# Kernel tuning notes

Measured on AMD Instinct MI355X. Metric: run time of the kernel, lower is better.

The kernel has to match this reference:

```python
import jax, jax.numpy as jnp
import numpy as np

NPOINT = 1024
RADIUS = 0.2
NSAMPLE = 64
BN_EPS = 1e-5


def setup_inputs() -> dict:
    key = jax.random.key(0)
    ks = jax.random.split(key, 16)
    B, N = 8, 8192
    inp = {
        "xyz": jax.random.normal(ks[0], (B, 3, N), jnp.float32),
        "points": jax.random.normal(ks[1], (B, 3, N), jnp.float32),
        "seed_inds": jax.random.randint(ks[2], (B, N), 0, N),
    }
    chans = [6, 64, 64, 128]
    for i in range(3):
        cin, cout = chans[i], chans[i + 1]
        kk = jax.random.split(ks[3 + i], 3)
        inp[f"w{i}"] = jax.random.normal(kk[0], (cout, cin), jnp.float32) / np.sqrt(cin)
        inp[f"b{i}"] = jnp.zeros((cout,), jnp.float32)
        inp[f"g{i}"] = jnp.ones((cout,), jnp.float32)
        inp[f"be{i}"] = jnp.zeros((cout,), jnp.float32)
        inp[f"m{i}"] = jax.random.normal(kk[1], (cout,), jnp.float32) * 0.1
        inp[f"v{i}"] = jax.random.uniform(kk[2], (cout,), jnp.float32, 0.5, 1.5)
    return inp


def _fps(xyz, npoint):
    # xyz: [B, N, 3]. Deterministic start at index 0 (torch uses a random start).
    B, N, _ = xyz.shape

    def step(carry, _):
        dist, far = carry
        cent = jnp.take_along_axis(xyz, far[:, None, None], axis=1)  # [B,1,3]
        d = jnp.sum((xyz - cent) ** 2, -1)                           # [B,N]
        dist = jnp.minimum(dist, d)
        nxt = jnp.argmax(dist, -1)
        return (dist, nxt), far

    init = (jnp.full((B, N), 1e10, xyz.dtype), jnp.zeros((B,), jnp.int32))
    _, idxs = jax.lax.scan(step, init, None, length=npoint)
    return idxs.T  # [B, npoint]


def _sqdist(src, dst):
    # src [B,S,3], dst [B,N,3] -> [B,S,N]
    d = -2.0 * jnp.einsum("bsc,bnc->bsn", src, dst)
    d += jnp.sum(src ** 2, -1)[:, :, None]
    d += jnp.sum(dst ** 2, -1)[:, None, :]
    return d


def _gather(pts, idx):
    # pts [B,N,C], idx [B,S,K] -> [B,S,K,C]
    B, S, K = idx.shape
    flat = jnp.take_along_axis(pts, idx.reshape(B, S * K, 1), axis=1)
    return flat.reshape(B, S, K, pts.shape[-1])


def _forward(xyz, points, seed_inds, layers):
    xyz_t = xyz.transpose(0, 2, 1)      # [B,N,3]
    pts_t = points.transpose(0, 2, 1)   # [B,N,D]
    B, N, _ = xyz_t.shape

    fps_idx = _fps(xyz_t, NPOINT)                                   # [B,S]
    new_seed = jnp.take_along_axis(seed_inds, fps_idx.astype(seed_inds.dtype), axis=1)
    new_xyz = jnp.take_along_axis(xyz_t, fps_idx[:, :, None], axis=1)  # [B,S,3]

    # ball query via sort trick (same math as torch module)
    sq = _sqdist(new_xyz, xyz_t)                                    # [B,S,N]
    gi = jnp.where(sq > RADIUS ** 2, N, jnp.arange(N, dtype=jnp.int32)[None, None, :])
    gi = jnp.sort(gi, axis=-1)[:, :, :NSAMPLE]                      # [B,S,K]
    first = gi[:, :, :1]
    gi = jnp.where(gi == N, first, gi)

    gxyz = _gather(xyz_t, gi) - new_xyz[:, :, None, :]              # [B,S,K,3]
    gpts = _gather(pts_t, gi)                                       # [B,S,K,D]
    feat = jnp.concatenate([gxyz, gpts], -1)                        # [B,S,K,3+D]

    for (w, b, g, be, m, v) in layers:
        feat = jnp.einsum("bskc,oc->bsko", feat, w) + b             # 1x1 conv
        feat = (feat - m) * (g / jnp.sqrt(v + BN_EPS)) + be         # BN (inference)
        feat = jax.nn.relu(feat)

    new_points = jnp.max(feat, axis=2).transpose(0, 2, 1)           # [B,Cout,S]
    return new_xyz.transpose(0, 2, 1), new_points, new_seed


def reference(xyz, points, seed_inds,
              w0, b0, g0, be0, m0, v0,
              w1, b1, g1, be1, m1, v1,
              w2, b2, g2, be2, m2, v2):
    layers = [(w0, b0, g0, be0, m0, v0),
              (w1, b1, g1, be1, m1, v1),
              (w2, b2, g2, be2, m2, v2)]
    return _forward(xyz, points, seed_inds, layers)
```

## Files before the change

kernel.cpp:

```cpp
#include <hip/hip_runtime.h>

#define B_ 8
#define N_ 8192
#define S_ 1024
#define NS_ 64

typedef float v2f __attribute__((ext_vector_type(2)));
typedef unsigned long long u64;

#define OUT0 0
#define OUT1 24576
#define OUT2 1073152

template <int CTRL>
static __device__ __forceinline__ float dpp_max_step(float v) {
    int o = __builtin_amdgcn_update_dpp(__float_as_int(v), __float_as_int(v),
                                        CTRL, 0xf, 0xf, false);
    return fmaxf(v, __int_as_float(o));
}
static __device__ __forceinline__ float wave_max_to_lane63(float v) {
    v = dpp_max_step<0x111>(v);
    v = dpp_max_step<0x112>(v);
    v = dpp_max_step<0x114>(v);
    v = dpp_max_step<0x118>(v);
    v = dpp_max_step<0x142>(v);
    v = dpp_max_step<0x143>(v);
    return v;
}
static __device__ __forceinline__ float wave_max_f32(float v) {
    v = wave_max_to_lane63(v);
    return __int_as_float(__builtin_amdgcn_readlane(__float_as_int(v), 63));
}
template <int CTRL>
static __device__ __forceinline__ unsigned dpp_umin_step(unsigned v) {
    unsigned o = (unsigned)__builtin_amdgcn_update_dpp((int)v, (int)v,
                                                       CTRL, 0xf, 0xf, false);
    return v < o ? v : o;
}
static __device__ __forceinline__ unsigned wave_min_u32(unsigned v) {
    v = dpp_umin_step<0x111>(v);
    v = dpp_umin_step<0x112>(v);
    v = dpp_umin_step<0x114>(v);
    v = dpp_umin_step<0x118>(v);
    v = dpp_umin_step<0x142>(v);
    v = dpp_umin_step<0x143>(v);
    return (unsigned)__builtin_amdgcn_readlane((int)v, 63);
}

#define FPS_T 512
#define FPS_J 8

__global__ __launch_bounds__(FPS_T, 1) void fps_kernel(const float* __restrict__ xyz,
                                                       float* out) {
    const int b = blockIdx.x;
    const int t = threadIdx.x;
    const int lane = t & 63;
    const float* X = xyz + b * 3 * N_;

    v2f px2[FPS_J], py2[FPS_J], pz2[FPS_J], dist2[FPS_J];
#pragma unroll
    for (int j = 0; j < FPS_J; ++j) {
        int n = t + 1024 * j;
        px2[j] = (v2f){X[n], X[n + 512]};
        py2[j] = (v2f){X[N_ + n], X[N_ + n + 512]};
        pz2[j] = (v2f){X[2 * N_ + n], X[2 * N_ + n + 512]};
        dist2[j] = (v2f){1e10f, 1e10f};
    }

    __shared__ u64 pairs[2];
    if (t == 0) { pairs[0] = 0ull; pairs[1] = 0ull; }
    __syncthreads();

    float* oseed = out + OUT2 + b * S_;

    int ci = 0;
    float c0 = X[0], c1 = X[N_], c2 = X[2 * N_];

    for (int step = 0; step < S_; ++step) {
        if (t == 0) oseed[step] = __int_as_float(ci);

        v2f mv = (v2f){-1.0f, -1.0f};
        {
#pragma clang fp contract(off)
            v2f c0v = (v2f){c0, c0};
            v2f c1v = (v2f){c1, c1};
            v2f c2v = (v2f){c2, c2};
#pragma unroll
            for (int j = 0; j < FPS_J; ++j) {
                v2f e0 = px2[j] - c0v;
                v2f e1 = py2[j] - c1v;
                v2f e2 = pz2[j] - c2v;
                v2f q0 = e0 * e0;
                v2f q1 = e1 * e1;
                v2f q2 = e2 * e2;
                v2f d  = (q0 + q1) + q2;
                v2f dm = __builtin_elementwise_min(dist2[j], d);
                dist2[j] = dm;
                mv = __builtin_elementwise_max(mv, dm);
            }
        }
        float m = fmaxf(mv.x, mv.y);

        float wmax = wave_max_f32(m);

        unsigned mask = 0u;
#pragma unroll
        for (int j = 0; j < FPS_J; ++j) {
            if (dist2[j].x == wmax) mask |= (1u << (2 * j));
            if (dist2[j].y == wmax) mask |= (1u << (2 * j + 1));
        }
        unsigned cand = 0xffffffffu;
        if (mask) {
            int bit = __ffs(mask) - 1;
            cand = (unsigned)(t + (bit << 9));
        }
        unsigned widx = wave_min_u32(cand);

        if (lane == 0) {
            u64 pv = ((u64)(step + 1) << 45) |
                     ((u64)__float_as_uint(wmax) << 13) |
                     (u64)(8191u - widx);
            atomicMax(&pairs[(step + 1) & 1], pv);
        }
        __syncthreads();

        u64 p = pairs[(step + 1) & 1];
        ci = 8191 - (int)(p & 0x1fffull);
        int cu = __builtin_amdgcn_readfirstlane(ci);
        c0 = X[cu];
        c1 = X[N_ + cu];
        c2 = X[2 * N_ + cu];
    }
}

__global__ __launch_bounds__(256) void gather_kernel(const float* __restrict__ xyz,
                                                     const int* __restrict__ seed,
                                                     float* out) {
    int t = blockIdx.x * 256 + threadIdx.x;
    int b = t >> 10, s = t & 1023;
    int idx = __float_as_int(out[OUT2 + t]) & 8191;
    const float* X = xyz + b * 3 * N_;
    float x = X[idx], y = X[N_ + idx], z = X[2 * N_ + idx];
    out[OUT0 + (b * 3 + 0) * S_ + s] = x;
    out[OUT0 + (b * 3 + 1) * S_ + s] = y;
    out[OUT0 + (b * 3 + 2) * S_ + s] = z;
    out[OUT2 + t] = (float)seed[b * N_ + idx];
}

__global__ __launch_bounds__(256) void ballquery_kernel(const float* __restrict__ xyz,
                                                        float* out) {
    int wid = threadIdx.x >> 6, lane = threadIdx.x & 63;
    int sg = blockIdx.x * 4 + wid;
    int b = sg >> 10, s = sg & 1023;
    const float* X = xyz + b * 3 * N_;
    float c0 = out[OUT0 + (b * 3 + 0) * S_ + s];
    float c1 = out[OUT0 + (b * 3 + 1) * S_ + s];
    float c2 = out[OUT0 + (b * 3 + 2) * S_ + s];
    float* G = out + OUT1 + (b * 128) * S_ + s;

    int cnt = 0, first = 0;
    for (int base = 0; base < N_ && cnt < NS_; base += 128) {
        int n0 = base + lane;
        int n1 = base + 64 + lane;
        float x0 = X[n0], y0 = X[N_ + n0], z0 = X[2 * N_ + n0];
        float x1 = X[n1], y1 = X[N_ + n1], z1 = X[2 * N_ + n1];
        float e0 = x0 - c0, e1 = y0 - c1, e2 = z0 - c2;
        float d0 = fmaf(e2, e2, fmaf(e1, e1, e0 * e0));
        float f0 = x1 - c0, f1 = y1 - c1, f2 = z1 - c2;
        float d1 = fmaf(f2, f2, fmaf(f1, f1, f0 * f0));

        u64 mask0 = __ballot(d0 <= 0.04f);
        if (mask0) {
            if (cnt == 0) first = base + __ffsll(mask0) - 1;
            int pos = cnt + (int)__popcll(mask0 & ((1ull << lane) - 1ull));
            if ((d0 <= 0.04f) && pos < NS_) G[pos * S_] = __int_as_float(n0);
            cnt += (int)__popcll(mask0);
        }
        u64 mask1 = __ballot(d1 <= 0.04f);
        if (mask1) {
            if (cnt == 0) first = base + 64 + __ffsll(mask1) - 1;
            int pos = cnt + (int)__popcll(mask1 & ((1ull << lane) - 1ull));
            if ((d1 <= 0.04f) && pos < NS_) G[pos * S_] = __int_as_float(n1);
            cnt += (int)__popcll(mask1);
        }
    }
    if (lane >= cnt && lane < NS_) G[lane * S_] = __int_as_float(first);
}

__global__ __launch_bounds__(256) void mlp_kernel(
    const float* __restrict__ xyz, const float* __restrict__ pts,
    const float* __restrict__ w0, const float* __restrict__ b0,
    const float* __restrict__ g0, const float* __restrict__ be0,
    const float* __restrict__ m0, const float* __restrict__ v0,
    const float* __restrict__ w1, const float* __restrict__ b1,
    const float* __restrict__ g1, const float* __restrict__ be1,
    const float* __restrict__ m1, const float* __restrict__ v1,
    const float* __restrict__ w2, const float* __restrict__ b2,
    const float* __restrict__ g2, const float* __restrict__ be2,
    const float* __restrict__ m2, const float* __restrict__ v2,
    float* out) {
    const int sg = blockIdx.x;
    const int b = sg >> 10, s = sg & 1023;
    const int t = threadIdx.x;
    const int lane = t & 63;
    const int wq = __builtin_amdgcn_readfirstlane(t >> 6);

    __shared__ float f0[64 * 9];
    __shared__ float bufA[64 * 65];
    __shared__ float bufB[64 * 65];
    __shared__ float scs[256], ofs[256];

    {
        float sc, of;
        if (t < 64) {
            int c = t;
            sc = g0[c] / sqrtf(v0[c] + 1e-5f);
            of = (b0[c] - m0[c]) * sc + be0[c];
        } else if (t < 128) {
            int c = t - 64;
            sc = g1[c] / sqrtf(v1[c] + 1e-5f);
            of = (b1[c] - m1[c]) * sc + be1[c];
        } else {
            int c = t - 128;
            sc = g2[c] / sqrtf(v2[c] + 1e-5f);
            of = (b2[c] - m2[c]) * sc + be2[c];
        }
        scs[t] = sc;
        ofs[t] = of;
    }

    if (t < 64) {
        int gidx = __float_as_int(out[OUT1 + (b * 128 + t) * S_ + s]) & 8191;
        const float* X = xyz + b * 3 * N_;
        const float* P = pts + b * 3 * N_;
        float cx = out[OUT0 + (b * 3 + 0) * S_ + s];
        float cy = out[OUT0 + (b * 3 + 1) * S_ + s];
        float cz = out[OUT0 + (b * 3 + 2) * S_ + s];
        f0[t * 9 + 0] = X[gidx] - cx;
        f0[t * 9 + 1] = X[N_ + gidx] - cy;
        f0[t * 9 + 2] = X[2 * N_ + gidx] - cz;
        f0[t * 9 + 3] = P[gidx];
        f0[t * 9 + 4] = P[N_ + gidx];
        f0[t * 9 + 5] = P[2 * N_ + gidx];
    }
    __syncthreads();

    {
        float in[6];
#pragma unroll
        for (int c = 0; c < 6; ++c) in[c] = f0[lane * 9 + c];
#pragma unroll 1
        for (int i = 0; i < 16; i += 4) {
            int o = wq * 16 + i;
            float a0 = 0.f, a1 = 0.f, a2 = 0.f, a3 = 0.f;
#pragma unroll
            for (int c = 0; c < 6; ++c) {
                float rc = in[c];
                a0 = fmaf(rc, w0[(o + 0) * 6 + c], a0);
                a1 = fmaf(rc, w0[(o + 1) * 6 + c], a1);
                a2 = fmaf(rc, w0[(o + 2) * 6 + c], a2);
                a3 = fmaf(rc, w0[(o + 3) * 6 + c], a3);
            }
            bufA[lane * 65 + o + 0] = fmaxf(fmaf(a0, scs[o + 0], ofs[o + 0]), 0.f);
            bufA[lane * 65 + o + 1] = fmaxf(fmaf(a1, scs[o + 1], ofs[o + 1]), 0.f);
            bufA[lane * 65 + o + 2] = fmaxf(fmaf(a2, scs[o + 2], ofs[o + 2]), 0.f);
            bufA[lane * 65 + o + 3] = fmaxf(fmaf(a3, scs[o + 3], ofs[o + 3]), 0.f);
        }
    }
    __syncthreads();

    {
        float r[64];
#pragma unroll
        for (int c = 0; c < 64; ++c) r[c] = bufA[lane * 65 + c];
#pragma unroll 1
        for (int i = 0; i < 16; i += 4) {
            int o = wq * 16 + i;
            float a0 = 0.f, a1 = 0.f, a2 = 0.f, a3 = 0.f;
#pragma unroll
            for (int c = 0; c < 64; ++c) {
                float rc = r[c];
                a0 = fmaf(rc, w1[(o + 0) * 64 + c], a0);
                a1 = fmaf(rc, w1[(o + 1) * 64 + c], a1);
                a2 = fmaf(rc, w1[(o + 2) * 64 + c], a2);
                a3 = fmaf(rc, w1[(o + 3) * 64 + c], a3);
            }
            bufB[lane * 65 + o + 0] = fmaxf(fmaf(a0, scs[64 + o + 0], ofs[64 + o + 0]), 0.f);
            bufB[lane * 65 + o + 1] = fmaxf(fmaf(a1, scs[64 + o + 1], ofs[64 + o + 1]), 0.f);
            bufB[lane * 65 + o + 2] = fmaxf(fmaf(a2, scs[64 + o + 2], ofs[64 + o + 2]), 0.f);
            bufB[lane * 65 + o + 3] = fmaxf(fmaf(a3, scs[64 + o + 3], ofs[64 + o + 3]), 0.f);
        }
    }
    __syncthreads();

    {
        float r[64];
#pragma unroll
        for (int c = 0; c < 64; ++c) r[c] = bufB[lane * 65 + c];
#pragma unroll 1
        for (int i = 0; i < 32; i += 4) {
            int o = wq * 32 + i;
            float a0 = 0.f, a1 = 0.f, a2 = 0.f, a3 = 0.f;
#pragma unroll
            for (int c = 0; c < 64; ++c) {
                float rc = r[c];
                a0 = fmaf(rc, w2[(o + 0) * 64 + c], a0);
                a1 = fmaf(rc, w2[(o + 1) * 64 + c], a1);
                a2 = fmaf(rc, w2[(o + 2) * 64 + c], a2);
                a3 = fmaf(rc, w2[(o + 3) * 64 + c], a3);
            }
            float y0 = wave_max_to_lane63(fmaxf(fmaf(a0, scs[128 + o + 0], ofs[128 + o + 0]), 0.f));
            float y1 = wave_max_to_lane63(fmaxf(fmaf(a1, scs[128 + o + 1], ofs[128 + o + 1]), 0.f));
            float y2 = wave_max_to_lane63(fmaxf(fmaf(a2, scs[128 + o + 2], ofs[128 + o + 2]), 0.f));
            float y3 = wave_max_to_lane63(fmaxf(fmaf(a3, scs[128 + o + 3], ofs[128 + o + 3]), 0.f));
            if (lane == 63) {
                out[OUT1 + (b * 128 + o + 0) * S_ + s] = y0;
                out[OUT1 + (b * 128 + o + 1) * S_ + s] = y1;
                out[OUT1 + (b * 128 + o + 2) * S_ + s] = y2;
                out[OUT1 + (b * 128 + o + 3) * S_ + s] = y3;
            }
        }
    }
}

extern "C" void kernel_launch(void* const* d_in, const int* in_sizes, int n_in,
                              void* d_out, int out_size, void* d_ws, size_t ws_size,
                              hipStream_t stream) {
    const float* xyz  = (const float*)d_in[0];
    const float* pts  = (const float*)d_in[1];
    const int*   seed = (const int*)d_in[2];
    const float* w0 = (const float*)d_in[3];
    const float* b0 = (const float*)d_in[4];
    const float* g0 = (const float*)d_in[5];
    const float* be0 = (const float*)d_in[6];
    const float* m0 = (const float*)d_in[7];
    const float* v0 = (const float*)d_in[8];
    const float* w1 = (const float*)d_in[9];
    const float* b1 = (const float*)d_in[10];
    const float* g1 = (const float*)d_in[11];
    const float* be1 = (const float*)d_in[12];
    const float* m1 = (const float*)d_in[13];
    const float* v1 = (const float*)d_in[14];
    const float* w2 = (const float*)d_in[15];
    const float* b2 = (const float*)d_in[16];
    const float* g2 = (const float*)d_in[17];
    const float* be2 = (const float*)d_in[18];
    const float* m2 = (const float*)d_in[19];
    const float* v2 = (const float*)d_in[20];
    float* out = (float*)d_out;
    (void)d_ws; (void)ws_size;

    fps_kernel<<<dim3(B_), dim3(FPS_T), 0, stream>>>(xyz, out);
    gather_kernel<<<dim3(8192 / 256), dim3(256), 0, stream>>>(xyz, seed, out);
    ballquery_kernel<<<dim3(2048), dim3(256), 0, stream>>>(xyz, out);
    mlp_kernel<<<dim3(8192), dim3(256), 0, stream>>>(xyz, pts,
        w0, b0, g0, be0, m0, v0,
        w1, b1, g1, be1, m1, v1,
        w2, b2, g2, be2, m2, v2,
        out);
}
```

Baseline: 1.433 ms.

## Fuse FPS, ball query and MLP into one persistent kernel with flag-based overlap

Adds a persistent fused kernel in which 8 blocks run farthest point sampling and publish progress through release/acquire flags every 64 centroids. The other 248 blocks poll those flags and do ball query, gather and the 3-layer MLP for each finished centroid, so this work overlaps the long serial FPS phase instead of waiting for it. FPS now writes centroid coordinates directly, which removes the separate gather kernel. The design relies on all 256 blocks being co-resident and on workspace being available; otherwise it falls back to the multi-kernel path.

Result: slower. 2.639 ms (+84.2%).

```diff
diff --git a/kernel.cpp b/kernel.cpp
--- a/kernel.cpp
+++ b/kernel.cpp
@@ -50,6 +50,280 @@
 #define FPS_T 512
 #define FPS_J 8
 
+__global__ __launch_bounds__(512, 1) void fused_kernel(
+    const float* __restrict__ xyz, const float* __restrict__ pts,
+    const int* __restrict__ seed,
+    const float* __restrict__ w0, const float* __restrict__ b0,
+    const float* __restrict__ g0, const float* __restrict__ be0,
+    const float* __restrict__ m0, const float* __restrict__ v0,
+    const float* __restrict__ w1, const float* __restrict__ b1,
+    const float* __restrict__ g1, const float* __restrict__ be1,
+    const float* __restrict__ m1, const float* __restrict__ v1,
+    const float* __restrict__ w2, const float* __restrict__ b2,
+    const float* __restrict__ g2, const float* __restrict__ be2,
+    const float* __restrict__ m2, const float* __restrict__ v2,
+    float* out, int* flags) {
+
+    __shared__ u64 pairs[2];
+    __shared__ float f0[64 * 9];
+    __shared__ float bufA[64 * 65];
+    __shared__ float bufB[64 * 65];
+    __shared__ float scs[256], ofs[256];
+    __shared__ int gis[64];
+
+    const int t = threadIdx.x;
+    const int lane = t & 63;
+
+    if (blockIdx.x < 8) {
+        const int b = blockIdx.x;
+        const float* X = xyz + b * 3 * N_;
+
+        v2f px2[FPS_J], py2[FPS_J], pz2[FPS_J], dist2[FPS_J];
+#pragma unroll
+        for (int j = 0; j < FPS_J; ++j) {
+            int n = t + 1024 * j;
+            px2[j] = (v2f){X[n], X[n + 512]};
+            py2[j] = (v2f){X[N_ + n], X[N_ + n + 512]};
+            pz2[j] = (v2f){X[2 * N_ + n], X[2 * N_ + n + 512]};
+            dist2[j] = (v2f){1e10f, 1e10f};
+        }
+
+        if (t == 0) { pairs[0] = 0ull; pairs[1] = 0ull; }
+        __syncthreads();
+
+        float* oseed = out + OUT2 + b * S_;
+
+        int ci = 0;
+        float c0 = X[0], c1 = X[N_], c2 = X[2 * N_];
+
+        for (int step = 0; step < S_; ++step) {
+            if (t == 0) oseed[step] = __int_as_float(ci);
+            if (t < 3) {
+                float cv = (t == 0) ? c0 : (t == 1) ? c1 : c2;
+                out[OUT0 + (b * 3 + t) * S_ + step] = cv;
+            }
+
+            v2f mv = (v2f){-1.0f, -1.0f};
+            {
+#pragma clang fp contract(off)
+                v2f c0v = (v2f){c0, c0};
+                v2f c1v = (v2f){c1, c1};
+                v2f c2v = (v2f){c2, c2};
+#pragma unroll
+                for (int j = 0; j < FPS_J; ++j) {
+                    v2f e0 = px2[j] - c0v;
+                    v2f e1 = py2[j] - c1v;
+                    v2f e2 = pz2[j] - c2v;
+                    v2f q0 = e0 * e0;
+                    v2f q1 = e1 * e1;
+                    v2f q2 = e2 * e2;
+                    v2f d  = (q0 + q1) + q2;
+                    v2f dm = __builtin_elementwise_min(dist2[j], d);
+                    dist2[j] = dm;
+                    mv = __builtin_elementwise_max(mv, dm);
+                }
+            }
+            float m = fmaxf(mv.x, mv.y);
+            float wmax = wave_max_f32(m);
+
+            unsigned mask = 0u;
+#pragma unroll
+            for (int j = 0; j < FPS_J; ++j) {
+                if (dist2[j].x == wmax) mask |= (1u << (2 * j));
+                if (dist2[j].y == wmax) mask |= (1u << (2 * j + 1));
+            }
+            unsigned cand = 0xffffffffu;
+            if (mask) {
+                int bit = __ffs(mask) - 1;
+                cand = (unsigned)(t + (bit << 9));
+            }
+            unsigned widx = wave_min_u32(cand);
+
+            if (lane == 0) {
+                u64 pv = ((u64)(step + 1) << 45) |
+                         ((u64)__float_as_uint(wmax) << 13) |
+                         (u64)(8191u - widx);
+                atomicMax(&pairs[(step + 1) & 1], pv);
+            }
+            __syncthreads();
+
+            u64 p = pairs[(step + 1) & 1];
+            ci = 8191 - (int)(p & 0x1fffull);
+            int cu = __builtin_amdgcn_readfirstlane(ci);
+            c0 = X[cu];
+            c1 = X[N_ + cu];
+            c2 = X[2 * N_ + cu];
+
+            if ((step & 63) == 63 && t == 0) {
+                __hip_atomic_store(&flags[b], step + 1, __ATOMIC_RELEASE,
+                                   __HIP_MEMORY_SCOPE_AGENT);
+            }
+        }
+    } else {
+        const int wq = __builtin_amdgcn_readfirstlane(t >> 6);
+
+        if (t < 256) {
+            float sc, of;
+            if (t < 64) {
+                int c = t;
+                sc = g0[c] / sqrtf(v0[c] + 1e-5f);
+                of = (b0[c] - m0[c]) * sc + be0[c];
+            } else if (t < 128) {
+                int c = t - 64;
+                sc = g1[c] / sqrtf(v1[c] + 1e-5f);
+                of = (b1[c] - m1[c]) * sc + be1[c];
+            } else {
+                int c = t - 128;
+                sc = g2[c] / sqrtf(v2[c] + 1e-5f);
+                of = (b2[c] - m2[c]) * sc + be2[c];
+            }
+            scs[t] = sc;
+            ofs[t] = of;
+        }
+        __syncthreads();
+
+        for (int sg = (int)blockIdx.x - 8; sg < B_ * S_; sg += 248) {
+            const int b = sg >> 10, s = sg & 1023;
+            const int want = s + 1;
+
+            while (__hip_atomic_load(&flags[b], __ATOMIC_ACQUIRE,
+                                     __HIP_MEMORY_SCOPE_AGENT) < want) {
+                __builtin_amdgcn_s_sleep(8);
+            }
+            __syncthreads();
+
+            const float* X = xyz + b * 3 * N_;
+            float cx = out[OUT0 + (b * 3 + 0) * S_ + s];
+            float cy = out[OUT0 + (b * 3 + 1) * S_ + s];
+            float cz = out[OUT0 + (b * 3 + 2) * S_ + s];
+
+            if (t < 64) {
+                int cnt = 0, first = 0;
+                for (int base = 0; base < N_ && cnt < NS_; base += 128) {
+                    int n0 = base + lane;
+                    int n1 = base + 64 + lane;
+                    float x0 = X[n0], y0 = X[N_ + n0], z0 = X[2 * N_ + n0];
+                    float x1 = X[n1], y1 = X[N_ + n1], z1 = X[2 * N_ + n1];
+                    float e0 = x0 - cx, e1 = y0 - cy, e2 = z0 - cz;
+                    float d0 = fmaf(e2, e2, fmaf(e1, e1, e0 * e0));
+                    float q0 = x1 - cx, q1 = y1 - cy, q2 = z1 - cz;
+                    float d1 = fmaf(q2, q2, fmaf(q1, q1, q0 * q0));
+
+                    u64 m0b = __ballot(d0 <= 0.04f);
+                    if (m0b) {
+                        if (cnt == 0) first = base + __ffsll(m0b) - 1;
+                        int pos = cnt + (int)__popcll(m0b & ((1ull << lane) - 1ull));
+                        if ((d0 <= 0.04f) && pos < NS_) gis[pos] = n0;
+                        cnt += (int)__popcll(m0b);
+                    }
+                    u64 m1b = __ballot(d1 <= 0.04f);
+                    if (m1b) {
+                        if (cnt == 0) first = base + 64 + __ffsll(m1b) - 1;
+                        int pos = cnt + (int)__popcll(m1b & ((1ull << lane) - 1ull));
+                        if ((d1 <= 0.04f) && pos < NS_) gis[pos] = n1;
+                        cnt += (int)__popcll(m1b);
+                    }
+                }
+                if (lane >= cnt && lane < NS_) gis[lane] = first;
+            } else if (t == 64) {
+                int sidx = __float_as_int(out[OUT2 + b * S_ + s]) & 8191;
+                out[OUT2 + b * S_ + s] = (float)seed[b * N_ + sidx];
+            }
+            __syncthreads();
+
+            if (t < 64) {
+                int gidx = gis[t] & 8191;
+                const float* P = pts + b * 3 * N_;
+                f0[t * 9 + 0] = X[gidx] - cx;
+                f0[t * 9 + 1] = X[N_ + gidx] - cy;
+                f0[t * 9 + 2] = X[2 * N_ + gidx] - cz;
+                f0[t * 9 + 3] = P[gidx];
+                f0[t * 9 + 4] = P[N_ + gidx];
+                f0[t * 9 + 5] = P[2 * N_ + gidx];
+            }
+            __syncthreads();
+
+            {
+                float in[6];
+#pragma unroll
+                for (int c = 0; c < 6; ++c) in[c] = f0[lane * 9 + c];
+#pragma unroll 1
+                for (int i = 0; i < 8; i += 4) {
+                    int o = wq * 8 + i;
+                    float a0 = 0.f, a1 = 0.f, a2 = 0.f, a3 = 0.f;
+#pragma unroll
+                    for (int c = 0; c < 6; ++c) {
+                        float rc = in[c];
+                        a0 = fmaf(rc, w0[(o + 0) * 6 + c], a0);
+                        a1 = fmaf(rc, w0[(o + 1) * 6 + c], a1);
+                        a2 = fmaf(rc, w0[(o + 2) * 6 + c], a2);
+                        a3 = fmaf(rc, w0[(o + 3) * 6 + c], a3);
+                    }
+                    bufA[lane * 65 + o + 0] = fmaxf(fmaf(a0, scs[o + 0], ofs[o + 0]), 0.f);
+                    bufA[lane * 65 + o + 1] = fmaxf(fmaf(a1, scs[o + 1], ofs[o + 1]), 0.f);
+                    bufA[lane * 65 + o + 2] = fmaxf(fmaf(a2, scs[o + 2], ofs[o + 2]), 0.f);
+                    bufA[lane * 65 + o + 3] = fmaxf(fmaf(a3, scs[o + 3], ofs[o + 3]), 0.f);
+                }
+            }
+            __syncthreads();
+
+            {
+                float r[64];
+#pragma unroll
+                for (int c = 0; c < 64; ++c) r[c] = bufA[lane * 65 + c];
+#pragma unroll 1
+                for (int i = 0; i < 8; i += 4) {
+                    int o = wq * 8 + i;
+                    float a0 = 0.f, a1 = 0.f, a2 = 0.f, a3 = 0.f;
+#pragma unroll
+                    for (int c = 0; c < 64; ++c) {
+                        float rc = r[c];
+                        a0 = fmaf(rc, w1[(o + 0) * 64 + c], a0);
+                        a1 = fmaf(rc, w1[(o + 1) * 64 + c], a1);
+                        a2 = fmaf(rc, w1[(o + 2) * 64 + c], a2);
+                        a3 = fmaf(rc, w1[(o + 3) * 64 + c], a3);
+                    }
+                    bufB[lane * 65 + o + 0] = fmaxf(fmaf(a0, scs[64 + o + 0], ofs[64 + o + 0]), 0.f);
+                    bufB[lane * 65 + o + 1] = fmaxf(fmaf(a1, scs[64 + o + 1], ofs[64 + o + 1]), 0.f);
+                    bufB[lane * 65 + o + 2] = fmaxf(fmaf(a2, scs[64 + o + 2], ofs[64 + o + 2]), 0.f);
+                    bufB[lane * 65 + o + 3] = fmaxf(fmaf(a3, scs[64 + o + 3], ofs[64 + o + 3]), 0.f);
+                }
+            }
+            __syncthreads();
+
+            {
+                float r[64];
+#pragma unroll
+                for (int c = 0; c < 64; ++c) r[c] = bufB[lane * 65 + c];
+#pragma unroll 1
+                for (int i = 0; i < 16; i += 4) {
+                    int o = wq * 16 + i;
+                    float a0 = 0.f, a1 = 0.f, a2 = 0.f, a3 = 0.f;
+#pragma unroll
+                    for (int c = 0; c < 64; ++c) {
+                        float rc = r[c];
+                        a0 = fmaf(rc, w2[(o + 0) * 64 + c], a0);
+                        a1 = fmaf(rc, w2[(o + 1) * 64 + c], a1);
+                        a2 = fmaf(rc, w2[(o + 2) * 64 + c], a2);
+                        a3 = fmaf(rc, w2[(o + 3) * 64 + c], a3);
+                    }
+                    float y0 = wave_max_to_lane63(fmaxf(fmaf(a0, scs[128 + o + 0], ofs[128 + o + 0]), 0.f));
+                    float y1 = wave_max_to_lane63(fmaxf(fmaf(a1, scs[128 + o + 1], ofs[128 + o + 1]), 0.f));
+                    float y2 = wave_max_to_lane63(fmaxf(fmaf(a2, scs[128 + o + 2], ofs[128 + o + 2]), 0.f));
+                    float y3 = wave_max_to_lane63(fmaxf(fmaf(a3, scs[128 + o + 3], ofs[128 + o + 3]), 0.f));
+                    if (lane == 63) {
+                        out[OUT1 + (b * 128 + o + 0) * S_ + s] = y0;
+                        out[OUT1 + (b * 128 + o + 1) * S_ + s] = y1;
+                        out[OUT1 + (b * 128 + o + 2) * S_ + s] = y2;
+                        out[OUT1 + (b * 128 + o + 3) * S_ + s] = y3;
+                    }
+                }
+            }
+            __syncthreads();
+        }
+    }
+}
+
 __global__ __launch_bounds__(FPS_T, 1) void fps_kernel(const float* __restrict__ xyz,
                                                        float* out) {
     const int b = blockIdx.x;
@@ -66,19 +340,18 @@
         pz2[j] = (v2f){X[2 * N_ + n], X[2 * N_ + n + 512]};
         dist2[j] = (v2f){1e10f, 1e10f};
     }
-
     __shared__ u64 pairs[2];
     if (t == 0) { pairs[0] = 0ull; pairs[1] = 0ull; }
     __syncthreads();
-
     float* oseed = out + OUT2 + b * S_;
-
     int ci = 0;
     float c0 = X[0], c1 = X[N_], c2 = X[2 * N_];
-
     for (int step = 0; step < S_; ++step) {
         if (t == 0) oseed[step] = __int_as_float(ci);
-
+        if (t < 3) {
+            float cv = (t == 0) ? c0 : (t == 1) ? c1 : c2;
+            out[OUT0 + (b * 3 + t) * S_ + step] = cv;
+        }
         v2f mv = (v2f){-1.0f, -1.0f};
         {
 #pragma clang fp contract(off)
@@ -100,9 +373,7 @@
             }
         }
         float m = fmaxf(mv.x, mv.y);
-
         float wmax = wave_max_f32(m);
-
         unsigned mask = 0u;
 #pragma unroll
         for (int j = 0; j < FPS_J; ++j) {
@@ -115,7 +386,6 @@
             cand = (unsigned)(t + (bit << 9));
         }
         unsigned widx = wave_min_u32(cand);
-
         if (lane == 0) {
             u64 pv = ((u64)(step + 1) << 45) |
                      ((u64)__float_as_uint(wmax) << 13) |
@@ -123,7 +393,6 @@
             atomicMax(&pairs[(step + 1) & 1], pv);
         }
         __syncthreads();
-
         u64 p = pairs[(step + 1) & 1];
         ci = 8191 - (int)(p & 0x1fffull);
         int cu = __builtin_amdgcn_readfirstlane(ci);
@@ -133,17 +402,11 @@
     }
 }
 
-__global__ __launch_bounds__(256) void gather_kernel(const float* __restrict__ xyz,
-                                                     const int* __restrict__ seed,
-                                                     float* out) {
+__global__ __launch_bounds__(256) void seedconv_kernel(const int* __restrict__ seed,
+                                                       float* out) {
     int t = blockIdx.x * 256 + threadIdx.x;
-    int b = t >> 10, s = t & 1023;
+    int b = t >> 10;
     int idx = __float_as_int(out[OUT2 + t]) & 8191;
-    const float* X = xyz + b * 3 * N_;
-    float x = X[idx], y = X[N_ + idx], z = X[2 * N_ + idx];
-    out[OUT0 + (b * 3 + 0) * S_ + s] = x;
-    out[OUT0 + (b * 3 + 1) * S_ + s] = y;
-    out[OUT0 + (b * 3 + 2) * S_ + s] = z;
     out[OUT2 + t] = (float)seed[b * N_ + idx];
 }
 
@@ -157,7 +420,6 @@
     float c1 = out[OUT0 + (b * 3 + 1) * S_ + s];
     float c2 = out[OUT0 + (b * 3 + 2) * S_ + s];
     float* G = out + OUT1 + (b * 128) * S_ + s;
-
     int cnt = 0, first = 0;
     for (int base = 0; base < N_ && cnt < NS_; base += 128) {
         int n0 = base + lane;
@@ -166,22 +428,21 @@
         float x1 = X[n1], y1 = X[N_ + n1], z1 = X[2 * N_ + n1];
         float e0 = x0 - c0, e1 = y0 - c1, e2 = z0 - c2;
         float d0 = fmaf(e2, e2, fmaf(e1, e1, e0 * e0));
-        float f0 = x1 - c0, f1 = y1 - c1, f2 = z1 - c2;
-        float d1 = fmaf(f2, f2, fmaf(f1, f1, f0 * f0));
-
-        u64 mask0 = __ballot(d0 <= 0.04f);
-        if (mask0) {
-            if (cnt == 0) first = base + __ffsll(mask0) - 1;
-            int pos = cnt + (int)__popcll(mask0 & ((1ull << lane) - 1ull));
+        float q0 = x1 - c0, q1 = y1 - c1, q2 = z1 - c2;
+        float d1 = fmaf(q2, q2, fmaf(q1, q1, q0 * q0));
+        u64 m0b = __ballot(d0 <= 0.04f);
+        if (m0b) {
+            if (cnt == 0) first = base + __ffsll(m0b) - 1;
+            int pos = cnt + (int)__popcll(m0b & ((1ull << lane) - 1ull));
             if ((d0 <= 0.04f) && pos < NS_) G[pos * S_] = __int_as_float(n0);
-            cnt += (int)__popcll(mask0);
-        }
-        u64 mask1 = __ballot(d1 <= 0.04f);
-        if (mask1) {
-            if (cnt == 0) first = base + 64 + __ffsll(mask1) - 1;
-            int pos = cnt + (int)__popcll(mask1 & ((1ull << lane) - 1ull));
+            cnt += (int)__popcll(m0b);
+        }
+        u64 m1b = __ballot(d1 <= 0.04f);
+        if (m1b) {
+            if (cnt == 0) first = base + 64 + __ffsll(m1b) - 1;
+            int pos = cnt + (int)__popcll(m1b & ((1ull << lane) - 1ull));
             if ((d1 <= 0.04f) && pos < NS_) G[pos * S_] = __int_as_float(n1);
-            cnt += (int)__popcll(mask1);
+            cnt += (int)__popcll(m1b);
         }
     }
     if (lane >= cnt && lane < NS_) G[lane * S_] = __int_as_float(first);
@@ -348,14 +609,23 @@
     const float* m2 = (const float*)d_in[19];
     const float* v2 = (const float*)d_in[20];
     float* out = (float*)d_out;
-    (void)d_ws; (void)ws_size;
-
-    fps_kernel<<<dim3(B_), dim3(FPS_T), 0, stream>>>(xyz, out);
-    gather_kernel<<<dim3(8192 / 256), dim3(256), 0, stream>>>(xyz, seed, out);
-    ballquery_kernel<<<dim3(2048), dim3(256), 0, stream>>>(xyz, out);
-    mlp_kernel<<<dim3(8192), dim3(256), 0, stream>>>(xyz, pts,
-        w0, b0, g0, be0, m0, v0,
-        w1, b1, g1, be1, m1, v1,
-        w2, b2, g2, be2, m2, v2,
-        out);
-}
+
+    if (ws_size >= 64) {
+        int* flags = (int*)d_ws;
+        hipMemsetAsync(flags, 0, 64, stream);
+        fused_kernel<<<dim3(256), dim3(512), 0, stream>>>(xyz, pts, seed,
+            w0, b0, g0, be0, m0, v0,
+            w1, b1, g1, be1, m1, v1,
+            w2, b2, g2, be2, m2, v2,
+            out, flags);
+    } else {
+        fps_kernel<<<dim3(B_), dim3(FPS_T), 0, stream>>>(xyz, out);
+        seedconv_kernel<<<dim3(8192 / 256), dim3(256), 0, stream>>>(seed, out);
+        ballquery_kernel<<<dim3(2048), dim3(256), 0, stream>>>(xyz, out);
+        mlp_kernel<<<dim3(8192), dim3(256), 0, stream>>>(xyz, pts,
+            w0, b0, g0, be0, m0, v0,
+            w1, b1, g1, be1, m1, v1,
+            w2, b2, g2, be2, m2, v2,
+            out);
+    }
+}
```

## Use bf16 MFMA for MLP layers 1 and 2 with per-wave row tiles

Applied to the files above, without the earlier changes.

Replaces the scalar FMA loops of the second and third 1x1 conv layers with 16x16x32 bf16 MFMA instructions. Activations are stored as bf16 in LDS and weights are converted to bf16 on the fly. Each wave now owns 16 sample rows instead of a slice of output channels, so the layer-1 to layer-2 handoff needs no block barrier and the max-pool is done per wave through shuffles plus a small LDS reduction. This trades fp32 accuracy for bf16 precision, and the weight conversion is repeated in every block.

After: 1.381 ms. -3.6%, faster.

```diff
diff --git a/kernel.cpp b/kernel.cpp
--- a/kernel.cpp
+++ b/kernel.cpp
@@ -7,6 +7,8 @@
 
 typedef float v2f __attribute__((ext_vector_type(2)));
 typedef unsigned long long u64;
+typedef short bf16x8 __attribute__((ext_vector_type(8)));
+typedef float f32x4 __attribute__((ext_vector_type(4)));
 
 #define OUT0 0
 #define OUT1 24576
@@ -18,17 +20,13 @@
                                         CTRL, 0xf, 0xf, false);
     return fmaxf(v, __int_as_float(o));
 }
-static __device__ __forceinline__ float wave_max_to_lane63(float v) {
+static __device__ __forceinline__ float wave_max_f32(float v) {
     v = dpp_max_step<0x111>(v);
     v = dpp_max_step<0x112>(v);
     v = dpp_max_step<0x114>(v);
     v = dpp_max_step<0x118>(v);
     v = dpp_max_step<0x142>(v);
     v = dpp_max_step<0x143>(v);
-    return v;
-}
-static __device__ __forceinline__ float wave_max_f32(float v) {
-    v = wave_max_to_lane63(v);
     return __int_as_float(__builtin_amdgcn_readlane(__float_as_int(v), 63));
 }
 template <int CTRL>
@@ -45,6 +43,11 @@
     v = dpp_umin_step<0x142>(v);
     v = dpp_umin_step<0x143>(v);
     return (unsigned)__builtin_amdgcn_readlane((int)v, 63);
+}
+
+static __device__ __forceinline__ short f2bf(float f) {
+    unsigned u = __float_as_uint(f);
+    return (short)((u + 0x7FFFu + ((u >> 16) & 1u)) >> 16);
 }
 
 #define FPS_T 512
@@ -100,7 +103,6 @@
             }
         }
         float m = fmaxf(mv.x, mv.y);
-
         float wmax = wave_max_f32(m);
 
         unsigned mask = 0u;
@@ -204,10 +206,13 @@
     const int t = threadIdx.x;
     const int lane = t & 63;
     const int wq = __builtin_amdgcn_readfirstlane(t >> 6);
+    const int ln = lane & 15;
+    const int quad = (lane >> 4) & 3;
 
     __shared__ float f0[64 * 9];
-    __shared__ float bufA[64 * 65];
-    __shared__ float bufB[64 * 65];
+    __shared__ short featA[64 * 72];
+    __shared__ short featB[64 * 72];
+    __shared__ float wmaxs[4 * 132];
     __shared__ float scs[256], ofs[256];
 
     {
@@ -261,65 +266,81 @@
                 a2 = fmaf(rc, w0[(o + 2) * 6 + c], a2);
                 a3 = fmaf(rc, w0[(o + 3) * 6 + c], a3);
             }
-            bufA[lane * 65 + o + 0] = fmaxf(fmaf(a0, scs[o + 0], ofs[o + 0]), 0.f);
-            bufA[lane * 65 + o + 1] = fmaxf(fmaf(a1, scs[o + 1], ofs[o + 1]), 0.f);
-            bufA[lane * 65 + o + 2] = fmaxf(fmaf(a2, scs[o + 2], ofs[o + 2]), 0.f);
-            bufA[lane * 65 + o + 3] = fmaxf(fmaf(a3, scs[o + 3], ofs[o + 3]), 0.f);
+            featA[lane * 72 + o + 0] = f2bf(fmaxf(fmaf(a0, scs[o + 0], ofs[o + 0]), 0.f));
+            featA[lane * 72 + o + 1] = f2bf(fmaxf(fmaf(a1, scs[o + 1], ofs[o + 1]), 0.f));
+            featA[lane * 72 + o + 2] = f2bf(fmaxf(fmaf(a2, scs[o + 2], ofs[o + 2]), 0.f));
+            featA[lane * 72 + o + 3] = f2bf(fmaxf(fmaf(a3, scs[o + 3], ofs[o + 3]), 0.f));
         }
     }
     __syncthreads();
 
+    const int arow = 16 * wq + ln;
+
     {
-        float r[64];
-#pragma unroll
-        for (int c = 0; c < 64; ++c) r[c] = bufA[lane * 65 + c];
-#pragma unroll 1
-        for (int i = 0; i < 16; i += 4) {
-            int o = wq * 16 + i;
-            float a0 = 0.f, a1 = 0.f, a2 = 0.f, a3 = 0.f;
-#pragma unroll
-            for (int c = 0; c < 64; ++c) {
-                float rc = r[c];
-                a0 = fmaf(rc, w1[(o + 0) * 64 + c], a0);
-                a1 = fmaf(rc, w1[(o + 1) * 64 + c], a1);
-                a2 = fmaf(rc, w1[(o + 2) * 64 + c], a2);
-                a3 = fmaf(rc, w1[(o + 3) * 64 + c], a3);
-            }
-            bufB[lane * 65 + o + 0] = fmaxf(fmaf(a0, scs[64 + o + 0], ofs[64 + o + 0]), 0.f);
-            bufB[lane * 65 + o + 1] = fmaxf(fmaf(a1, scs[64 + o + 1], ofs[64 + o + 1]), 0.f);
-            bufB[lane * 65 + o + 2] = fmaxf(fmaf(a2, scs[64 + o + 2], ofs[64 + o + 2]), 0.f);
-            bufB[lane * 65 + o + 3] = fmaxf(fmaf(a3, scs[64 + o + 3], ofs[64 + o + 3]), 0.f);
+        bf16x8 a1f[2];
+#pragma unroll
+        for (int ks = 0; ks < 2; ++ks)
+            a1f[ks] = *(const bf16x8*)&featA[arow * 72 + ks * 32 + quad * 8];
+
+#pragma unroll
+        for (int nt = 0; nt < 4; ++nt) {
+            f32x4 acc = {0.f, 0.f, 0.f, 0.f};
+#pragma unroll
+            for (int ks = 0; ks < 2; ++ks) {
+                const float* wr = w1 + (nt * 16 + ln) * 64 + ks * 32 + quad * 8;
+                float4 p = *(const float4*)wr;
+                float4 q = *(const float4*)(wr + 4);
+                bf16x8 bf = {f2bf(p.x), f2bf(p.y), f2bf(p.z), f2bf(p.w),
+                             f2bf(q.x), f2bf(q.y), f2bf(q.z), f2bf(q.w)};
+                acc = __builtin_amdgcn_mfma_f32_16x16x32_bf16(a1f[ks], bf, acc, 0, 0, 0);
+            }
+            int o = nt * 16 + ln;
+            float sc = scs[64 + o], of = ofs[64 + o];
+#pragma unroll
+            for (int reg = 0; reg < 4; ++reg) {
+                float y = fmaxf(fmaf(acc[reg], sc, of), 0.f);
+                featB[(16 * wq + quad * 4 + reg) * 72 + o] = f2bf(y);
+            }
+        }
+    }
+
+    {
+        bf16x8 a2f[2];
+#pragma unroll
+        for (int ks = 0; ks < 2; ++ks)
+            a2f[ks] = *(const bf16x8*)&featB[arow * 72 + ks * 32 + quad * 8];
+
+#pragma unroll
+        for (int nt = 0; nt < 8; ++nt) {
+            f32x4 acc = {0.f, 0.f, 0.f, 0.f};
+#pragma unroll
+            for (int ks = 0; ks < 2; ++ks) {
+                const float* wr = w2 + (nt * 16 + ln) * 64 + ks * 32 + quad * 8;
+                float4 p = *(const float4*)wr;
+                float4 q = *(const float4*)(wr + 4);
+                bf16x8 bf = {f2bf(p.x), f2bf(p.y), f2bf(p.z), f2bf(p.w),
+                             f2bf(q.x), f2bf(q.y), f2bf(q.z), f2bf(q.w)};
+                acc = __builtin_amdgcn_mfma_f32_16x16x32_bf16(a2f[ks], bf, acc, 0, 0, 0);
+            }
+            int o = nt * 16 + ln;
+            float sc = scs[128 + o], of = ofs[128 + o];
+            float m = -1.f;
+#pragma unroll
+            for (int reg = 0; reg < 4; ++reg) {
+                float y = fmaxf(fmaf(acc[reg], sc, of), 0.f);
+                m = fmaxf(m, y);
+            }
+            m = fmaxf(m, __shfl_xor(m, 16, 64));
+            m = fmaxf(m, __shfl_xor(m, 32, 64));
+            if (lane < 16) wmaxs[wq * 132 + o] = m;
         }
     }
     __syncthreads();
 
-    {
-        float r[64];
-#pragma unroll
-        for (int c = 0; c < 64; ++c) r[c] = bufB[lane * 65 + c];
-#pragma unroll 1
-        for (int i = 0; i < 32; i += 4) {
-            int o = wq * 32 + i;
-            float a0 = 0.f, a1 = 0.f, a2 = 0.f, a3 = 0.f;
-#pragma unroll
-            for (int c = 0; c < 64; ++c) {
-                float rc = r[c];
-                a0 = fmaf(rc, w2[(o + 0) * 64 + c], a0);
-                a1 = fmaf(rc, w2[(o + 1) * 64 + c], a1);
-                a2 = fmaf(rc, w2[(o + 2) * 64 + c], a2);
-                a3 = fmaf(rc, w2[(o + 3) * 64 + c], a3);
-            }
-            float y0 = wave_max_to_lane63(fmaxf(fmaf(a0, scs[128 + o + 0], ofs[128 + o + 0]), 0.f));
-            float y1 = wave_max_to_lane63(fmaxf(fmaf(a1, scs[128 + o + 1], ofs[128 + o + 1]), 0.f));
-            float y2 = wave_max_to_lane63(fmaxf(fmaf(a2, scs[128 + o + 2], ofs[128 + o + 2]), 0.f));
-            float y3 = wave_max_to_lane63(fmaxf(fmaf(a3, scs[128 + o + 3], ofs[128 + o + 3]), 0.f));
-            if (lane == 63) {
-                out[OUT1 + (b * 128 + o + 0) * S_ + s] = y0;
-                out[OUT1 + (b * 128 + o + 1) * S_ + s] = y1;
-                out[OUT1 + (b * 128 + o + 2) * S_ + s] = y2;
-                out[OUT1 + (b * 128 + o + 3) * S_ + s] = y3;
-            }
-        }
+    if (t < 128) {
+        float m = fmaxf(fmaxf(wmaxs[0 * 132 + t], wmaxs[1 * 132 + t]),
+                        fmaxf(wmaxs[2 * 132 + t], wmaxs[3 * 132 + t]));
+        out[OUT1 + (b * 128 + t) * S_ + s] = m;
     }
 }
 
```
